# Kernel optimization log

Hardware: AMD Instinct MI355X
Metric: run time of the kernel (lower is better)

The kernel has to match this reference:

```python
import jax, jax.numpy as jnp
import numpy as np
from jax import lax

DIM = 96
KS = 7
EPS = 1e-6


def setup_inputs() -> dict:
    key = jax.random.key(0)
    ks = jax.random.split(key, 12)
    N, C, H, W = 64, DIM, 56, 56
    s = 0.02
    x = jax.random.normal(ks[0], (N, C, H, W), dtype=jnp.float32)
    dw_w = jax.random.normal(ks[1], (C, 1, KS, KS), dtype=jnp.float32) * s  # depthwise, OIHW with I=1
    dw_b = jnp.zeros((C,), dtype=jnp.float32)
    ln_g = jnp.ones((C,), dtype=jnp.float32)
    ln_b = jnp.zeros((C,), dtype=jnp.float32)
    w1 = jax.random.normal(ks[2], (4 * C, C), dtype=jnp.float32) * s   # torch Linear weight [out,in]
    b1 = jnp.zeros((4 * C,), dtype=jnp.float32)
    grn_g = jnp.zeros((4 * C,), dtype=jnp.float32)  # GRN gamma/beta init to 0 as in ConvNeXtV2
    grn_b = jnp.zeros((4 * C,), dtype=jnp.float32)
    w2 = jax.random.normal(ks[3], (C, 4 * C), dtype=jnp.float32) * s
    b2 = jnp.zeros((C,), dtype=jnp.float32)
    return {"x": x, "dw_w": dw_w, "dw_b": dw_b, "ln_g": ln_g, "ln_b": ln_b,
            "w1": w1, "b1": b1, "grn_g": grn_g, "grn_b": grn_b, "w2": w2, "b2": b2}


def reference(x, dw_w, dw_b, ln_g, ln_b, w1, b1, grn_g, grn_b, w2, b2):
    C = x.shape[1]
    pad = KS // 2
    # 7x7 depthwise conv, NCHW
    y = lax.conv_general_dilated(x, dw_w, window_strides=(1, 1),
                                 padding=[(pad, pad), (pad, pad)],
                                 dimension_numbers=("NCHW", "OIHW", "NCHW"),
                                 feature_group_count=C)
    y = y + dw_b[None, :, None, None]
    y = jnp.transpose(y, (0, 2, 3, 1))  # [N,H,W,C]
    # channels-last LayerNorm, eps=1e-6
    mu = jnp.mean(y, axis=-1, keepdims=True)
    var = jnp.mean(jnp.square(y - mu), axis=-1, keepdims=True)
    y = (y - mu) * lax.rsqrt(var + EPS) * ln_g + ln_b
    # pwconv1 -> GELU (exact erf, torch default)
    y = jnp.einsum("nhwc,fc->nhwf", y, w1) + b1
    y = jax.nn.gelu(y, approximate=False)
    # GRN over spatial dims
    gx = jnp.sqrt(jnp.sum(jnp.square(y), axis=(1, 2), keepdims=True))  # [N,1,1,4C]
    nx = gx / (jnp.mean(gx, axis=-1, keepdims=True) + EPS)
    y = grn_g * (y * nx) + grn_b + y
    # pwconv2
    y = jnp.einsum("nhwf,cf->nhwc", y, w2) + b2
    y = jnp.transpose(y, (0, 3, 1, 2))  # back to NCHW
    # drop_path=0.0 -> identity; residual add
    return x + y
```

## Files before the change

kernel.cpp:

```cpp
#include <hip/hip_runtime.h>
#include <hip/hip_bf16.h>
#include <math.h>

#define HW   3136
#define NIMG 64
#define M_TOT (NIMG * HW)

typedef __attribute__((ext_vector_type(8))) short bf16x8_t;
typedef __attribute__((ext_vector_type(4))) float f32x4_t;
typedef __bf16 bf16x2v __attribute__((ext_vector_type(2)));

__device__ __forceinline__ unsigned short f2bf(float f) {
  union { float f; unsigned u; } v; v.f = f;
  unsigned r = v.u + 0x7FFFu + ((v.u >> 16) & 1u);
  return (unsigned short)(r >> 16);
}
__device__ __forceinline__ float bf2f(unsigned short h) {
  union { unsigned u; float f; } v; v.u = ((unsigned)h) << 16;
  return v.f;
}

__device__ __forceinline__ float dot2bf(unsigned a, unsigned b, float c) {
#if __has_builtin(__builtin_amdgcn_fdot2_f32_bf16)
  return __builtin_amdgcn_fdot2_f32_bf16(__builtin_bit_cast(bf16x2v, a),
                                         __builtin_bit_cast(bf16x2v, b), c, false);
#else
  return c + bf2f((unsigned short)(a & 0xffffu)) * bf2f((unsigned short)(b & 0xffffu))
           + bf2f((unsigned short)(a >> 16)) * bf2f((unsigned short)(b >> 16));
#endif
}

__device__ __forceinline__ int xcd_swz(int bid0) {
  return ((bid0 & 7) * 392) + (bid0 >> 3);
}

__global__ void k0_swz(const float* __restrict__ wsrc, unsigned short* __restrict__ bsw,
                       int N, int K) {
  int idx = blockIdx.x * 256 + threadIdx.x;
  int total = (N / 16) * (K / 32) * 64;
  if (idx >= total) return;
  int l  = idx & 63;
  int fi = idx >> 6;
  int KT = K / 32;
  int nt = fi / KT, kt = fi - nt * KT;
  int nn = nt * 16 + (l & 15);
  int kb = kt * 32 + (l >> 4) * 8;
  const float* src = wsrc + (size_t)nn * K + kb;
  unsigned short* dst = bsw + (size_t)idx * 8;
#pragma unroll
  for (int j = 0; j < 8; j++) dst[j] = f2bf(src[j]);
}

__global__ void k0_b2p(const float* __restrict__ w2, const float* __restrict__ grnb,
                       const float* __restrict__ b2, float* __restrict__ b2p) {
  int c = blockIdx.x * blockDim.x + threadIdx.x;
  if (c >= 96) return;
  float s = b2[c];
  const float* wr = w2 + (size_t)c * 384;
  for (int f = 0; f < 384; f++) s += grnb[f] * wr[f];
  b2p[c] = s;
}

__global__ void k0w(const float* __restrict__ dww, unsigned short* __restrict__ wswz) {
  int i = blockIdx.x * 256 + threadIdx.x;
  if (i >= 96 * 56) return;
  int ch = i / 56, rem = i - ch * 56, dy = rem >> 3, dx = rem & 7;
  wswz[i] = (dx < 7) ? f2bf(dww[ch * 49 + dy * 7 + dx]) : (unsigned short)0;
}

__global__ __launch_bounds__(256, 3) void k12f(
    const float* __restrict__ x, const unsigned short* __restrict__ wswz,
    const float* __restrict__ dwb, const float* __restrict__ lng,
    const float* __restrict__ lnb, const unsigned short* __restrict__ B1,
    const float* __restrict__ b1, unsigned char* __restrict__ y1f8,
    float* __restrict__ gx2) {
  __shared__ char smem[28928];
  float* lnp = (float*)smem;
  unsigned short* xsh = (unsigned short*)(smem + 768);
  unsigned short (*ts)[104] = (unsigned short(*)[104])(smem + 15616);

  const int t = threadIdx.x;
  const int bid = xcd_swz(blockIdx.x);
  const int n = bid / 49;
  const int tile = bid - n * 49;
  const int tr = tile / 7, tc = tile - tr * 7;
  const int h0 = tr * 8, w0 = tc * 8;

  if (t < 192) lnp[t] = (t < 96) ? lng[t] : lnb[t - 96];

  const int cch = t & 31, crow = t >> 5;
  const bool colInt = (tc >= 1) && (tc <= 5);
  const bool rowInt = (tr >= 1) && (tr <= 5);

  int g_r[7], g_ch[7], g_wb[7];
  bool g_hok[7];
#pragma unroll
  for (int k = 0; k < 7; k++) {
    int i = t + k * 256;
    int cq = i & 3;
    int rc = i >> 2;
    g_r[k] = rc % 14; g_ch[k] = rc / 14;
    g_wb[k] = w0 + cq * 4 - 3;
    g_hok[k] = (unsigned)(h0 + g_r[k] - 3) < 56u;
  }

  float4 raw[3][7];
#pragma unroll
  for (int cc = 0; cc < 3; cc++) {
#pragma unroll
    for (int k = 0; k < 7; k++) {
      const int h = h0 + g_r[k] - 3;
      const int wb = g_wb[k];
      const float* xb = x + (size_t)(n * 96 + cc * 32 + g_ch[k]) * HW + h * 56 + wb;
      float4 v;
      if (rowInt && colInt) {
        v = *(const float4*)xb;
      } else {
        v = make_float4(0.f, 0.f, 0.f, 0.f);
        if (g_hok[k]) {
          if (colInt) {
            v = *(const float4*)xb;
          } else {
            if ((unsigned)(wb + 0) < 56u) v.x = xb[0];
            if ((unsigned)(wb + 1) < 56u) v.y = xb[1];
            if ((unsigned)(wb + 2) < 56u) v.z = xb[2];
            if ((unsigned)(wb + 3) < 56u) v.w = xb[3];
          }
        }
      }
      raw[cc][k] = v;
    }
  }

#pragma unroll
  for (int cc = 0; cc < 3; cc++) {
    const int c0 = cc * 32;
    if (cc) __syncthreads();
#pragma unroll
    for (int k = 0; k < 7; k++) {
      float4 v = raw[cc][k];
      uint2 u;
      u.x = (unsigned)f2bf(v.x) | ((unsigned)f2bf(v.y) << 16);
      u.y = (unsigned)f2bf(v.z) | ((unsigned)f2bf(v.w) << 16);
      *(uint2*)&xsh[g_ch[k] * 232 + g_r[k] * 16 + (g_wb[k] - w0 + 3)] = u;
    }
    bf16x8_t wv[7];
#pragma unroll
    for (int dy = 0; dy < 7; dy++)
      wv[dy] = *(const bf16x8_t*)&wswz[(size_t)(c0 + cch) * 56 + dy * 8];
    const float bias = dwb[c0 + cch];
    __syncthreads();
    float acc[8];
#pragma unroll
    for (int j = 0; j < 8; j++) acc[j] = bias;
#pragma unroll
    for (int dy = 0; dy < 7; dy++) {
      const unsigned* pr = (const unsigned*)&xsh[cch * 232 + (crow + dy) * 16];
      uint4 pa = *(const uint4*)pr;
      uint4 pb = *(const uint4*)(pr + 4);
      unsigned p[8] = {pa.x, pa.y, pa.z, pa.w, pb.x, pb.y, pb.z, pb.w};
      unsigned q[7];
#pragma unroll
      for (int i = 0; i < 7; i++) q[i] = (p[i] >> 16) | (p[i + 1] << 16);
      const unsigned* wu = (const unsigned*)&wv[dy];
#pragma unroll
      for (int j = 0; j < 8; j += 2) {
        int b = j >> 1;
        acc[j] = dot2bf(wu[3], p[b + 3],
                 dot2bf(wu[2], p[b + 2],
                 dot2bf(wu[1], p[b + 1],
                 dot2bf(wu[0], p[b + 0], acc[j]))));
        acc[j + 1] = dot2bf(wu[3], q[b + 3],
                     dot2bf(wu[2], q[b + 2],
                     dot2bf(wu[1], q[b + 1],
                     dot2bf(wu[0], q[b + 0], acc[j + 1]))));
      }
    }
#pragma unroll
    for (int j = 0; j < 8; j++)
      ts[crow * 8 + j][c0 + cch] = f2bf(acc[j]);
  }
  __syncthreads();

  {
    const int px = t >> 2, q = t & 3;
    const unsigned onebf = 0x3F803F80u;
    unsigned vu[12];
    float s = 0.f, ss = 0.f;
#pragma unroll
    for (int j = 0; j < 12; j++) {
      vu[j] = *(const unsigned*)&ts[px][q * 24 + j * 2];
      s  = dot2bf(vu[j], onebf, s);
      ss = dot2bf(vu[j], vu[j], ss);
    }
    s  += __shfl_xor(s, 1);  s  += __shfl_xor(s, 2);
    ss += __shfl_xor(ss, 1); ss += __shfl_xor(ss, 2);
    float mu  = s * (1.f / 96.f);
    float var = ss * (1.f / 96.f) - mu * mu;
    float rs  = rsqrtf(var + 1e-6f);
#pragma unroll
    for (int j = 0; j < 12; j++) {
      int ch = q * 24 + j * 2;
      float v0 = bf2f((unsigned short)(vu[j] & 0xffffu));
      float v1 = bf2f((unsigned short)(vu[j] >> 16));
      float o0 = (v0 - mu) * rs * lnp[ch] + lnp[96 + ch];
      float o1 = (v1 - mu) * rs * lnp[ch + 1] + lnp[96 + ch + 1];
      *(unsigned*)&ts[px][ch] = (unsigned)f2bf(o0) | ((unsigned)f2bf(o1) << 16);
    }
  }
  __syncthreads();

  const int wv_ = t >> 6, l = t & 63;
  const int lg = l >> 4, lr = l & 15;
  bf16x8_t bfr[4][3];
#pragma unroll
  for (int nt = 0; nt < 4; nt++)
#pragma unroll
    for (int kc = 0; kc < 3; kc++)
      bfr[nt][kc] = *(const bf16x8_t*)&ts[nt * 16 + lr][kc * 32 + lg * 8];

#pragma unroll
  for (int ftl = 0; ftl < 6; ftl++) {
    const int ft = wv_ * 6 + ftl;
    bf16x8_t aw[3];
#pragma unroll
    for (int kc = 0; kc < 3; kc++)
      aw[kc] = *(const bf16x8_t*)(B1 + ((size_t)(ft * 3 + kc) * 64 + l) * 8);
    float4 bq = *(const float4*)(b1 + ft * 16 + lg * 4);
    f32x4_t acc[4];
#pragma unroll
    for (int nt = 0; nt < 4; nt++) acc[nt] = (f32x4_t){0.f, 0.f, 0.f, 0.f};
#pragma unroll
    for (int kc = 0; kc < 3; kc++)
#pragma unroll
      for (int nt = 0; nt < 4; nt++)
        acc[nt] = __builtin_amdgcn_mfma_f32_16x16x32_bf16(aw[kc], bfr[nt][kc], acc[nt], 0, 0, 0);
    float s2[4] = {0.f, 0.f, 0.f, 0.f};
    const int kt = wv_ * 3 + (ftl >> 1);
    const int jh = (ftl & 1) * 4;
#pragma unroll
    for (int nt = 0; nt < 4; nt++) {
      float g[4];
#pragma unroll
      for (int r = 0; r < 4; r++) {
        float v = acc[nt][r] + ((const float*)&bq)[r];
        float sq = v * v;
        float pe = fmaf(sq, -0.10295294f, -2.3021183f);
        float e  = __builtin_amdgcn_exp2f(v * pe);
        float gg = v * __builtin_amdgcn_rcpf(1.f + e);
        g[r] = gg;
        s2[r] += gg * gg;
      }
      unsigned p = (unsigned)__builtin_amdgcn_cvt_pk_fp8_f32(g[0], g[1], 0, false);
      p = (unsigned)__builtin_amdgcn_cvt_pk_fp8_f32(g[2], g[3], p, true);
      *(unsigned*)(y1f8 +
        (((size_t)(bid * 4 + nt) * 12 + kt) * 64 + l) * 8 + jh) = p;
    }
#pragma unroll
    for (int r = 0; r < 4; r++) {
      float v = s2[r];
      v += __shfl_xor(v, 1); v += __shfl_xor(v, 2);
      v += __shfl_xor(v, 4); v += __shfl_xor(v, 8);
      if (lr == 0)
        atomicAdd(gx2 + n * 384 + ft * 16 + lg * 4 + r, v);
    }
  }
}

__global__ __launch_bounds__(256) void k3_coefB(
    const float* __restrict__ gx2, const float* __restrict__ grng,
    const float* __restrict__ w2, unsigned char* __restrict__ B2s8) {
  __shared__ float red[256];
  __shared__ float cf[384];
  const int n = blockIdx.x, t = threadIdx.x;
  float s = 0.f;
  for (int f = t; f < 384; f += 256) {
    float g = sqrtf(gx2[n * 384 + f]);
    cf[f] = g; s += g;
  }
  red[t] = s; __syncthreads();
  for (int o = 128; o > 0; o >>= 1) {
    if (t < o) red[t] += red[t + o];
    __syncthreads();
  }
  float inv = 1.f / (red[0] * (1.f / 384.f) + 1e-6f);
  for (int f = t; f < 384; f += 256)
    cf[f] = 1.f + grng[f] * cf[f] * inv;
  __syncthreads();
  unsigned char* dstn = B2s8 + (size_t)n * 36864;
  for (int i = t; i < 4608; i += 256) {
    int fi = i >> 6, ll = i & 63;
    int kt = fi % 12, nt = fi / 12;
    int lg = ll >> 4, lr = ll & 15;
    int c  = nt * 16 + lr;
    int f0 = kt * 32 + lg * 4;
    const float* wr = w2 + (size_t)c * 384;
    float4 wa = *(const float4*)(wr + f0);
    float4 wb = *(const float4*)(wr + f0 + 16);
    float vv[8];
    vv[0] = wa.x * cf[f0 + 0];  vv[1] = wa.y * cf[f0 + 1];
    vv[2] = wa.z * cf[f0 + 2];  vv[3] = wa.w * cf[f0 + 3];
    vv[4] = wb.x * cf[f0 + 16]; vv[5] = wb.y * cf[f0 + 17];
    vv[6] = wb.z * cf[f0 + 18]; vv[7] = wb.w * cf[f0 + 19];
    unsigned p0 = (unsigned)__builtin_amdgcn_cvt_pk_fp8_f32(vv[0], vv[1], 0, false);
    p0 = (unsigned)__builtin_amdgcn_cvt_pk_fp8_f32(vv[2], vv[3], p0, true);
    unsigned p1 = (unsigned)__builtin_amdgcn_cvt_pk_fp8_f32(vv[4], vv[5], 0, false);
    p1 = (unsigned)__builtin_amdgcn_cvt_pk_fp8_f32(vv[6], vv[7], p1, true);
    uint2 o; o.x = p0; o.y = p1;
    *(uint2*)(dstn + (size_t)i * 8) = o;
  }
}

__global__ __launch_bounds__(256) void k4_gemm2(
    const unsigned char* __restrict__ y1f8, const unsigned char* __restrict__ B2s8,
    const float* __restrict__ b2p, const float* __restrict__ x,
    float* __restrict__ out) {
  __shared__ float zt[96][68];
  const int t  = threadIdx.x;
  const int wv = t >> 6, l = t & 63;
  const int lg = l >> 4, lr = l & 15;
  const int bid = xcd_swz(blockIdx.x);
  const int n = bid / 49;
  const int tile = bid - n * 49;
  const int tr = tile / 7, tc = tile - tr * 7;
  const unsigned char* Bn = B2s8 + (size_t)n * 36864;

  long af[12];
  const unsigned char* ap = y1f8 + ((size_t)(bid * 4 + wv) * 12) * 512 + l * 8;
#pragma unroll
  for (int kt = 0; kt < 12; kt++)
    af[kt] = *(const long*)(ap + kt * 512);

  f32x4_t acc[6];
#pragma unroll
  for (int i = 0; i < 6; i++) acc[i] = (f32x4_t){0.f, 0.f, 0.f, 0.f};
#pragma unroll
  for (int kt = 0; kt < 12; kt++) {
#pragma unroll
    for (int nt = 0; nt < 6; nt++) {
      long b = *(const long*)(Bn + ((size_t)(nt * 12 + kt) * 64 + l) * 8);
      acc[nt] = __builtin_amdgcn_mfma_f32_16x16x32_fp8_fp8(af[kt], b, acc[nt], 0, 0, 0);
    }
  }
#pragma unroll
  for (int nt = 0; nt < 6; nt++) {
    int c = nt * 16 + lr;
#pragma unroll
    for (int r = 0; r < 4; r++)
      zt[c][wv * 16 + lg * 4 + r] = acc[nt][r];
  }
  __syncthreads();
#pragma unroll
  for (int it = 0; it < 6; it++) {
    int id = t + it * 256;
    int c = id >> 4, q = id & 15;
    int row = q >> 1, jq = (q & 1) * 4;
    float4 z = *(const float4*)&zt[c][row * 8 + jq];
    size_t base = ((size_t)(n * 96 + c)) * HW + (size_t)(tr * 8 + row) * 56 + tc * 8 + jq;
    float4 xv = *(const float4*)(x + base);
    float bp = b2p[c];
    float4 o;
    o.x = xv.x + z.x + bp;
    o.y = xv.y + z.y + bp;
    o.z = xv.z + z.z + bp;
    o.w = xv.w + z.w + bp;
    *(float4*)(out + base) = o;
  }
}

extern "C" void kernel_launch(void* const* d_in, const int* in_sizes, int n_in,
                              void* d_out, int out_size, void* d_ws, size_t ws_size,
                              hipStream_t stream) {
  const float* x    = (const float*)d_in[0];
  const float* dww  = (const float*)d_in[1];
  const float* dwb  = (const float*)d_in[2];
  const float* lng  = (const float*)d_in[3];
  const float* lnb  = (const float*)d_in[4];
  const float* w1   = (const float*)d_in[5];
  const float* b1   = (const float*)d_in[6];
  const float* grng = (const float*)d_in[7];
  const float* grnb = (const float*)d_in[8];
  const float* w2   = (const float*)d_in[9];
  const float* b2   = (const float*)d_in[10];
  float* out = (float*)d_out;

  char* ws = (char*)d_ws;
  size_t off = 0;
  auto alloc = [&](size_t bytes) {
    char* p = ws + off;
    off += (bytes + 255) & ~(size_t)255;
    return p;
  };
  unsigned char*  y1f8 = (unsigned char*)alloc((size_t)M_TOT * 384);
  unsigned char*  B2s8 = (unsigned char*)alloc((size_t)64 * 36864);
  unsigned short* B1sw = (unsigned short*)alloc((size_t)384 * 96 * 2);
  unsigned short* wswz = (unsigned short*)alloc((size_t)96 * 56 * 2);
  float* gx2  = (float*)alloc((size_t)64 * 384 * 4);
  float* b2p  = (float*)alloc((size_t)96 * 4);
  if (off > ws_size) return;

  hipMemsetAsync(gx2, 0, 64 * 384 * 4, stream);
  k0_swz<<<18, 256, 0, stream>>>(w1, B1sw, 384, 96);
  k0_b2p<<<1, 128, 0, stream>>>(w2, grnb, b2, b2p);
  k0w<<<21, 256, 0, stream>>>(dww, wswz);
  k12f<<<3136, 256, 0, stream>>>(x, wswz, dwb, lng, lnb, B1sw, b1, y1f8, gx2);
  k3_coefB<<<64, 256, 0, stream>>>(gx2, grng, w2, B2s8);
  k4_gemm2<<<3136, 256, 0, stream>>>(y1f8, B2s8, b2p, x, out);
}
```

Before: 189.3 us.

## Give each wavefront private depthwise-conv channels to drop block barriers

The depthwise conv staging is restructured so each wavefront loads, converts and convolves its own 8 channels in a private shared-memory slice. This removes the block-wide __syncthreads between the staging and compute phases of each channel chunk. It also drops the up-front register prefetch of all three chunks (raw[3][7]), so global loads are no longer batched ahead of compute. That lowers register pressure but may expose more load latency. The result depends on wavefront-level lockstep for correctness within each slice, with no explicit barrier.

```diff
diff --git a/kernel.cpp b/kernel.cpp
--- a/kernel.cpp
+++ b/kernel.cpp
@@ -88,36 +88,36 @@
 
   if (t < 192) lnp[t] = (t < 96) ? lng[t] : lnb[t - 96];
 
-  const int cch = t & 31, crow = t >> 5;
+  const int wv_ = t >> 6, l = t & 63;
+  const int rch = l >> 3, crow = l & 7;
   const bool colInt = (tc >= 1) && (tc <= 5);
   const bool rowInt = (tr >= 1) && (tr <= 5);
-
-  int g_r[7], g_ch[7], g_wb[7];
-  bool g_hok[7];
+  unsigned short* xw = xsh + wv_ * 1856;
+
+  int s_ch[7], s_r[7], s_cq[7];
+  bool s_hok[7];
 #pragma unroll
   for (int k = 0; k < 7; k++) {
-    int i = t + k * 256;
-    int cq = i & 3;
-    int rc = i >> 2;
-    g_r[k] = rc % 14; g_ch[k] = rc / 14;
-    g_wb[k] = w0 + cq * 4 - 3;
-    g_hok[k] = (unsigned)(h0 + g_r[k] - 3) < 56u;
-  }
-
-  float4 raw[3][7];
-#pragma unroll
+    int slot = l + k * 64;
+    s_ch[k] = slot / 56;
+    int rem = slot - s_ch[k] * 56;
+    s_r[k] = rem >> 2; s_cq[k] = rem & 3;
+    s_hok[k] = (unsigned)(h0 + s_r[k] - 3) < 56u;
+  }
+
   for (int cc = 0; cc < 3; cc++) {
+    const int c0 = cc * 32;
 #pragma unroll
     for (int k = 0; k < 7; k++) {
-      const int h = h0 + g_r[k] - 3;
-      const int wb = g_wb[k];
-      const float* xb = x + (size_t)(n * 96 + cc * 32 + g_ch[k]) * HW + h * 56 + wb;
+      const int h = h0 + s_r[k] - 3;
+      const int wb = w0 + s_cq[k] * 4 - 3;
+      const float* xb = x + (size_t)(n * 96 + c0 + wv_ * 8 + s_ch[k]) * HW + h * 56 + wb;
       float4 v;
       if (rowInt && colInt) {
         v = *(const float4*)xb;
       } else {
         v = make_float4(0.f, 0.f, 0.f, 0.f);
-        if (g_hok[k]) {
+        if (s_hok[k]) {
           if (colInt) {
             v = *(const float4*)xb;
           } else {
@@ -128,41 +128,30 @@
           }
         }
       }
-      raw[cc][k] = v;
-    }
-  }
-
-#pragma unroll
-  for (int cc = 0; cc < 3; cc++) {
-    const int c0 = cc * 32;
-    if (cc) __syncthreads();
-#pragma unroll
-    for (int k = 0; k < 7; k++) {
-      float4 v = raw[cc][k];
       uint2 u;
       u.x = (unsigned)f2bf(v.x) | ((unsigned)f2bf(v.y) << 16);
       u.y = (unsigned)f2bf(v.z) | ((unsigned)f2bf(v.w) << 16);
-      *(uint2*)&xsh[g_ch[k] * 232 + g_r[k] * 16 + (g_wb[k] - w0 + 3)] = u;
-    }
-    bf16x8_t wv[7];
+      *(uint2*)&xw[s_ch[k] * 232 + s_r[k] * 16 + s_cq[k] * 4] = u;
+    }
+    const int mych = c0 + wv_ * 8 + rch;
+    bf16x8_t wvv[7];
 #pragma unroll
     for (int dy = 0; dy < 7; dy++)
-      wv[dy] = *(const bf16x8_t*)&wswz[(size_t)(c0 + cch) * 56 + dy * 8];
-    const float bias = dwb[c0 + cch];
-    __syncthreads();
+      wvv[dy] = *(const bf16x8_t*)&wswz[(size_t)mych * 56 + dy * 8];
+    const float bias = dwb[mych];
     float acc[8];
 #pragma unroll
     for (int j = 0; j < 8; j++) acc[j] = bias;
 #pragma unroll
     for (int dy = 0; dy < 7; dy++) {
-      const unsigned* pr = (const unsigned*)&xsh[cch * 232 + (crow + dy) * 16];
+      const unsigned* pr = (const unsigned*)&xw[rch * 232 + (crow + dy) * 16];
       uint4 pa = *(const uint4*)pr;
       uint4 pb = *(const uint4*)(pr + 4);
       unsigned p[8] = {pa.x, pa.y, pa.z, pa.w, pb.x, pb.y, pb.z, pb.w};
       unsigned q[7];
 #pragma unroll
       for (int i = 0; i < 7; i++) q[i] = (p[i] >> 16) | (p[i + 1] << 16);
-      const unsigned* wu = (const unsigned*)&wv[dy];
+      const unsigned* wu = (const unsigned*)&wvv[dy];
 #pragma unroll
       for (int j = 0; j < 8; j += 2) {
         int b = j >> 1;
@@ -178,7 +167,7 @@
     }
 #pragma unroll
     for (int j = 0; j < 8; j++)
-      ts[crow * 8 + j][c0 + cch] = f2bf(acc[j]);
+      ts[crow * 8 + j][mych] = f2bf(acc[j]);
   }
   __syncthreads();
 
@@ -210,7 +199,6 @@
   }
   __syncthreads();
 
-  const int wv_ = t >> 6, l = t & 63;
   const int lg = l >> 4, lr = l & 15;
   bf16x8_t bfr[4][3];
 #pragma unroll
```

After: 191.0 us. No clear change (+0.9%).
